# Performance work log

Measured on AMD Instinct MI355X. Metric: run time of the kernel, lower is better.

Reference implementation:

```python
import jax, jax.numpy as jnp
import numpy as np

DMODEL = 1024
NUM_HEADS = 16
HEAD_DIM = DMODEL // NUM_HEADS


def setup_inputs() -> dict:
    key = jax.random.key(0)
    k_x, k_wqkv, k_bqkv, k_wo, k_bo = jax.random.split(key, 5)
    B, T, D = 4, 2048, DMODEL
    s = 1.0 / np.sqrt(D)
    return {
        "x": jax.random.normal(k_x, (B, T, D), dtype=jnp.float32),
        "w_qkv": jax.random.uniform(k_wqkv, (D, 3 * D), dtype=jnp.float32, minval=-s, maxval=s),
        "b_qkv": jax.random.uniform(k_bqkv, (3 * D,), dtype=jnp.float32, minval=-s, maxval=s),
        "w_out": jax.random.uniform(k_wo, (D, D), dtype=jnp.float32, minval=-s, maxval=s),
        "b_out": jax.random.uniform(k_bo, (D,), dtype=jnp.float32, minval=-s, maxval=s),
    }


def reference(x, w_qkv, b_qkv, w_out, b_out):
    B, T, D = x.shape
    H, Hd = NUM_HEADS, HEAD_DIM
    qkv = x @ w_qkv + b_qkv                      # [B,T,3D]
    qkv = qkv.reshape(B, T, 3, H, Hd)
    q = jnp.transpose(qkv[:, :, 0], (0, 2, 1, 3))  # [B,H,T,Hd]
    k = jnp.transpose(qkv[:, :, 1], (0, 2, 1, 3))
    v = jnp.transpose(qkv[:, :, 2], (0, 2, 1, 3))
    scores = jnp.einsum("bhqd,bhkd->bhqk", q, k) / jnp.sqrt(jnp.float32(Hd))
    weights = jax.nn.softmax(scores, axis=-1)
    attn = jnp.einsum("bhqk,bhkd->bhqd", weights, v)  # [B,H,T,Hd]
    attn = jnp.transpose(attn, (0, 2, 1, 3)).reshape(B, T, D)
    return attn @ w_out + b_out
```

## Files before the change

### kernel.cpp

```cpp
#include <hip/hip_runtime.h>
#include <hip/hip_bf16.h>


typedef __bf16 bf16_t;
typedef __bf16 bf16x8 __attribute__((ext_vector_type(8)));
typedef float f32x4 __attribute__((ext_vector_type(4)));
typedef short short4v __attribute__((ext_vector_type(4)));

#if __has_builtin(__builtin_amdgcn_mfma_f32_16x16x16_bf16)
typedef __bf16 bf16x4 __attribute__((ext_vector_type(4)));
#define MFMA_PV(va, vb, c) __builtin_amdgcn_mfma_f32_16x16x16_bf16( \
    __builtin_bit_cast(bf16x4, (va)), __builtin_bit_cast(bf16x4, (vb)), (c), 0, 0, 0)
#else
#define MFMA_PV(va, vb, c) __builtin_amdgcn_mfma_f32_16x16x16bf16_1k((va), (vb), (c), 0, 0, 0)
#endif

#define DMODEL 1024
#define NH     16
#define HD     64
#define BATCH  4
#define SEQ    2048
#define NTOK   (BATCH * SEQ)
#define NOUT   (NTOK * DMODEL)
#define CEXP   0.1803368801111204f

__device__ __forceinline__ void async_ld16(void* lds, const void* g) {
  __builtin_amdgcn_global_load_lds(
      (const __attribute__((address_space(1))) void*)g,
      (__attribute__((address_space(3))) void*)lds, 16, 0, 0);
}

__global__ __launch_bounds__(256) void sniff_dtype(
    const uint4* __restrict__ x, int* __restrict__ flag,
    const void* __restrict__ sq, const void* __restrict__ so,
    float* __restrict__ dq, float* __restrict__ dofs) {
  int t = threadIdx.x;
  int nanish = 0, zc = 0;
  for (int j = 0; j < 4; ++j) {
    uint4 w = x[t + j * 256];
    unsigned u[4] = {w.x, w.y, w.z, w.w};
    for (int k = 0; k < 4; ++k) {
      unsigned lo = u[k] & 0xFFFFu, hi = u[k] >> 16;
      if ((lo & 0x7F80u) == 0x7F80u) nanish++;
      if ((hi & 0x7F80u) == 0x7F80u) nanish++;
      if (lo == 0) zc++;
      if (hi == 0) zc++;
    }
  }
  __shared__ int rn[256], rz[256];
  rn[t] = nanish; rz[t] = zc;
  __syncthreads();
  for (int s = 128; s > 0; s >>= 1) {
    if (t < s) { rn[t] += rn[t + s]; rz[t] += rz[t + s]; }
    __syncthreads();
  }
  const int f = (rn[0] > 4 || rz[0] > 2048) ? 1 : 0;
  if (t == 0) flag[0] = f;
  for (int j = 0; j < 16; ++j) {
    int i = j * 256 + t;
    if (i < 3072)
      dq[i] = f ? ((const float*)sq)[i] : (float)((const bf16_t*)sq)[i];
    else {
      int k = i - 3072;
      dofs[k] = f ? ((const float*)so)[k] : (float)((const bf16_t*)so)[k];
    }
  }
}

__global__ __launch_bounds__(256) void conv_and_transpose(
    const void* __restrict__ x, bf16_t* __restrict__ xb,
    const void* __restrict__ w0, bf16_t* __restrict__ out0,
    const void* __restrict__ w1, bf16_t* __restrict__ out1,
    const int* __restrict__ flag) {
  const int bb = blockIdx.x;
  if (bb < 4096) {
    int i = (bb * 256 + threadIdx.x) * 8;
    if (flag[0]) {
      const float4* s = (const float4*)((const float*)x + i);
      float4 a = s[0], b = s[1];
      bf16_t* o = xb + i;
      o[0] = (bf16_t)a.x; o[1] = (bf16_t)a.y; o[2] = (bf16_t)a.z; o[3] = (bf16_t)a.w;
      o[4] = (bf16_t)b.x; o[5] = (bf16_t)b.y; o[6] = (bf16_t)b.z; o[7] = (bf16_t)b.w;
    } else {
      *(uint4*)(xb + i) = *(const uint4*)((const bf16_t*)x + i);
    }
    return;
  }
  __shared__ bf16_t tile[32][33];
  const int idx = bb - 4096;
  const int bxT = idx & 127, byT = idx >> 7;
  const int tx = threadIdx.x & 31, ty = threadIdx.x >> 5;
  const bool second = bxT >= 96;
  const void* in = second ? w1 : w0;
  bf16_t* out = second ? out1 : out0;
  const int C = second ? 1024 : 3072;
  const int R = 1024;
  const int c0 = (second ? (bxT - 96) : bxT) * 32;
  const int r0 = byT * 32;
  if (flag[0]) {
    for (int i = 0; i < 4; ++i) {
      int r = ty + i * 8;
      tile[r][tx] = (bf16_t)((const float*)in)[(size_t)(r0 + r) * C + c0 + tx];
    }
  } else {
    for (int i = 0; i < 4; ++i) {
      int r = ty + i * 8;
      tile[r][tx] = ((const bf16_t*)in)[(size_t)(r0 + r) * C + c0 + tx];
    }
  }
  __syncthreads();
  for (int i = 0; i < 4; ++i) {
    int r = ty + i * 8;
    out[(size_t)(c0 + r) * R + r0 + tx] = tile[tx][r];
  }
}

template <int MODE>
__global__ __launch_bounds__(512) void gemm_v2(
    const bf16_t* __restrict__ A, const bf16_t* __restrict__ Bt,
    const float* __restrict__ bias, void* __restrict__ Cout,
    int M, int N, int K, bf16_t* __restrict__ vT,
    const int* __restrict__ flag) {
  __shared__ __align__(16) char smem[98304];
  char* lds = smem;
  const int t = threadIdx.x;
  const int wave = t >> 6, lane = t & 63;
  const int quad = lane >> 4, l16 = lane & 15;
  const int wr = wave >> 2, wc = wave & 3;
  const int lin = blockIdx.y * gridDim.x + blockIdx.x;
  const int xcd = lin & 7;
  const int slot = lin >> 3;
  const int Rrows = ((gridDim.x * gridDim.y) >> 3) / gridDim.x;
  const int CW = gridDim.x < 4 ? gridDim.x : 4;
  const int CB = CW * Rrows;
  const int chunk = slot / CB, within = slot % CB;
  const int bx = chunk * CW + within % CW;
  const int by = xcd * Rrows + within / CW;
  const int bM = by * 128, bN = bx * 256;

  const int srow = t >> 2;
  const int xr = ((srow >> 3) & 1) | (((srow >> 2) & 1) << 1);
  const int skl = ((t ^ xr) & 3) * 8;
  const size_t offA = (size_t)(bM + srow) * K + skl;
  const size_t offB = (size_t)(bN + srow) * K + skl;
  const size_t offB2 = offB + (size_t)128 * K;

#define STG(g) do {                                                            \
    const int tile_ = (g) >> 1, half_ = (g) & 1;                               \
    const int kk_ = tile_ * 64 + half_ * 32;                                   \
    char* base_ = lds + ((tile_ & 1) ? 49152 : 0);                             \
    async_ld16(base_ + half_ * 8192 + t * 16, A + offA + kk_);                 \
    async_ld16(base_ + 16384 + half_ * 16384 + t * 16, Bt + offB + kk_);       \
    async_ld16(base_ + 16384 + half_ * 16384 + 8192 + t * 16,                  \
               Bt + offB2 + kk_); } while (0)

  int aoff[4], boff[4];
#pragma unroll
  for (int mf = 0; mf < 4; ++mf) {
    int r = wr * 64 + mf * 16 + l16;
    aoff[mf] = ((r << 6) + (quad << 4)) ^ (((r & 8) << 1) | ((r & 4) << 3));
  }
#pragma unroll
  for (int nf = 0; nf < 4; ++nf) {
    int r = wc * 64 + nf * 16 + l16;
    boff[nf] = ((r << 6) + (quad << 4)) ^ (((r & 8) << 1) | ((r & 4) << 3));
  }

  f32x4 acc[4][4] = {};
  const int NT = K >> 6;

  STG(0); STG(1); STG(2);
  asm volatile("s_waitcnt vmcnt(6)" ::: "memory");
  __builtin_amdgcn_s_barrier();
  asm volatile("" ::: "memory");

#define PHASE(T, h) do {                                                       \
    const int bufo_ = ((T) & 1) * 49152;                                       \
    bf16x8 af[4], bf[4];                                                       \
    _Pragma("unroll") for (int i_ = 0; i_ < 4; ++i_)                           \
      af[i_] = *(const bf16x8*)(lds + bufo_ + (h) * 8192 + aoff[i_]);          \
    _Pragma("unroll") for (int j_ = 0; j_ < 4; ++j_)                           \
      bf[j_] = *(const bf16x8*)(lds + bufo_ + 16384 + (h) * 16384 + boff[j_]); \
    const int n_ = 2 * (T) + (h);                                              \
    if (n_ + 3 < 2 * NT) {                                                     \
      STG(n_ + 3);                                                             \
      asm volatile("s_waitcnt vmcnt(6)" ::: "memory");                         \
    } else if (n_ == 2 * NT - 3) {                                             \
      asm volatile("s_waitcnt vmcnt(3)" ::: "memory");                         \
    } else if (n_ == 2 * NT - 2) {                                             \
      asm volatile("s_waitcnt vmcnt(0)" ::: "memory");                         \
    }                                                                          \
    __builtin_amdgcn_s_barrier();                                              \
    asm volatile("" ::: "memory");                                             \
    __builtin_amdgcn_s_setprio(1);                                             \
    _Pragma("unroll") for (int i_ = 0; i_ < 4; ++i_)                           \
      { _Pragma("unroll") for (int j_ = 0; j_ < 4; ++j_)                       \
        acc[i_][j_] = __builtin_amdgcn_mfma_f32_16x16x32_bf16(                 \
            af[i_], bf[j_], acc[i_][j_], 0, 0, 0); }                           \
    __builtin_amdgcn_s_setprio(0);                                             \
    asm volatile("" ::: "memory");                                             \
    __builtin_amdgcn_s_barrier(); } while (0)

  for (int T = 0; T < NT; ++T) {
    PHASE(T, 0);
    PHASE(T, 1);
  }

  const bool f32out = (MODE == 1) && flag[0];
#pragma unroll
  for (int nf = 0; nf < 4; ++nf) {
    int col = bN + wc * 64 + nf * 16 + l16;
    float bv = bias[col];
#pragma unroll
    for (int mf = 0; mf < 4; ++mf) {
      int row0 = bM + wr * 64 + mf * 16 + quad * 4;
      if (MODE == 2 && col >= 2048) {
        int hh = (col - 2048) >> 6, dd = (col - 2048) & 63;
        bf16_t o4[4];
        for (int r = 0; r < 4; ++r) o4[r] = (bf16_t)(acc[mf][nf][r] + bv);
        size_t dst = ((((size_t)(row0 >> 11) * NH + hh) * HD + dd) << 11) | (row0 & 2047);
        *(uint2*)&vT[dst] = *(uint2*)o4;
      } else if (MODE == 2) {
        float scale = (col < 1024) ? CEXP : 1.0f;
        for (int r = 0; r < 4; ++r)
          ((bf16_t*)Cout)[(size_t)(row0 + r) * N + col] =
              (bf16_t)((acc[mf][nf][r] + bv) * scale);
      } else {
        for (int r = 0; r < 4; ++r) {
          float v = acc[mf][nf][r] + bv;
          if (f32out) ((float*)Cout)[(size_t)(row0 + r) * N + col] = v;
          else        ((bf16_t*)Cout)[(size_t)(row0 + r) * N + col] = (bf16_t)v;
        }
      }
    }
  }
#undef STG
#undef PHASE
}

__global__ __launch_bounds__(512) void attention_v12(
    const bf16_t* __restrict__ qkv, const bf16_t* __restrict__ vT,
    bf16_t* __restrict__ attn) {
  const int t = threadIdx.x;
  const int wave = t >> 6, lane = t & 63;
  const int quad = lane >> 4, l16 = lane & 15;
  const int bh = blockIdx.x, b = bh >> 4, h = bh & 15;
  const int qw = blockIdx.y * 256 + wave * 32;

  __shared__ bf16_t Kt[2][128 * 64];
  __shared__ bf16_t Vt[2][64 * 128];

  const bf16_t* qglob = qkv + (size_t)b * SEQ * 3072 + h * 64;
  const bf16_t* kglob = qglob + 1024;
  const bf16_t* vglob = vT + (size_t)bh * HD * SEQ;

  bf16x8 qf[2][2];
  for (int s = 0; s < 2; ++s) {
    const bf16_t* qrow = qglob + (size_t)(qw + s * 16 + l16) * 3072 + quad * 8;
    qf[s][0] = *(const bf16x8*)qrow;
    qf[s][1] = *(const bf16x8*)(qrow + 32);
  }

  f32x4 accO[2][4] = {};
  f32x4 lsum[2] = {};
  const short4v ones4 = {(short)0x3F80, (short)0x3F80, (short)0x3F80, (short)0x3F80};

  const int kRow = lane >> 3, kSlot = lane & 7;
  const int vRow = lane >> 4, vSlot = lane & 15;

  auto stageKV = [&](int buf, int kt) {
    for (int j = 0; j < 2; ++j) {
      int keyl = wave * 16 + j * 8 + kRow;
      int gc = kSlot ^ (keyl & 7);
      async_ld16((char*)Kt[buf] + (wave * 16 + j * 8) * 128,
                 kglob + (size_t)(kt + keyl) * 3072 + gc * 8);
    }
    for (int j = 0; j < 2; ++j) {
      int d = wave * 8 + j * 4 + vRow;
      int gc = vSlot ^ (d & 15);
      async_ld16((char*)Vt[buf] + (wave * 8 + j * 4) * 256,
                 vglob + (size_t)d * SEQ + kt + gc * 8);
    }
  };

  stageKV(0, 0);

  for (int ti = 0; ti < SEQ / 128; ++ti) {
    const int buf = ti & 1;
    __syncthreads();
    if (ti + 1 < SEQ / 128) stageKV(buf ^ 1, (ti + 1) * 128);

    const bf16_t* KtB = Kt[buf];
    const bf16_t* VtB = Vt[buf];

    for (int kb = 0; kb < 8; ++kb) {
      const bf16_t* kr = &KtB[(kb * 16 + l16) * 64];
      bf16x8 kf0 = *(const bf16x8*)(kr + ((quad ^ (l16 & 7)) * 8));
      bf16x8 kf1 = *(const bf16x8*)(kr + (((4 + quad) ^ (l16 & 7)) * 8));

      short4v pB[2];
      for (int s = 0; s < 2; ++s) {
        f32x4 z = {0.f, 0.f, 0.f, 0.f};
        f32x4 st = __builtin_amdgcn_mfma_f32_16x16x32_bf16(kf0, qf[s][0], z, 0, 0, 0);
        st = __builtin_amdgcn_mfma_f32_16x16x32_bf16(kf1, qf[s][1], st, 0, 0, 0);
        union { bf16_t hh[4]; short4v s4; } u;
        for (int r = 0; r < 4; ++r) {
          float p = __builtin_amdgcn_exp2f(st[r]);
          u.hh[r] = (bf16_t)p;
        }
        pB[s] = u.s4;
        lsum[s] = MFMA_PV(ones4, pB[s], lsum[s]);
      }

      const int chunkbase = kb * 2 + (quad >> 1);
      const int coff = (quad & 1) * 4;
      for (int db = 0; db < 4; ++db) {
        short4v vf = *(const short4v*)&VtB[(db * 16 + l16) * 128 +
                                           ((chunkbase ^ l16) * 8) + coff];
        for (int s = 0; s < 2; ++s)
          accO[s][db] = MFMA_PV(vf, pB[s], accO[s][db]);
      }
    }
  }

  for (int s = 0; s < 2; ++s) {
    float inv = 1.f / lsum[s][0];
    size_t tok = (size_t)b * SEQ + qw + s * 16 + l16;
    for (int db = 0; db < 4; ++db) {
      bf16_t o4[4];
      for (int r = 0; r < 4; ++r) o4[r] = (bf16_t)(accO[s][db][r] * inv);
      *(uint2*)&attn[tok * DMODEL + h * HD + db * 16 + quad * 4] = *(uint2*)o4;
    }
  }
}

extern "C" void kernel_launch(void* const* d_in, const int* in_sizes, int n_in,
                              void* d_out, int out_size, void* d_ws, size_t ws_size,
                              hipStream_t stream) {
  const void* x     = d_in[0];
  const void* w_qkv = d_in[1];
  const void* b_qkv = d_in[2];
  const void* w_out = d_in[3];
  const void* b_out = d_in[4];

  char* ws = (char*)d_ws;
  int*    flag  = (int*)ws;
  bf16_t* wqkvT = (bf16_t*)(ws + 4096);
  bf16_t* woutT = (bf16_t*)(ws + 6295552);
  float*  bqkvf = (float*)(ws + 8392704);
  float*  boutf = (float*)(ws + 8404992);
  bf16_t* qkv   = (bf16_t*)(ws + 8409088);
  bf16_t* xb    = (bf16_t*)(ws + 58740736);
  bf16_t* attn  = xb;
  bf16_t* vTbuf = (bf16_t*)(ws + 75517952);

  sniff_dtype<<<1, 256, 0, stream>>>((const uint4*)x, flag, b_qkv, b_out,
                                     bqkvf, boutf);

  conv_and_transpose<<<8192, 256, 0, stream>>>(x, xb, w_qkv, wqkvT, w_out, woutT,
                                               flag);

  gemm_v2<2><<<dim3(12, 64), 512, 0, stream>>>(
      xb, wqkvT, bqkvf, qkv, NTOK, 3072, 1024, vTbuf, flag);

  attention_v12<<<dim3(BATCH * NH, SEQ / 256), 512, 0, stream>>>(qkv, vTbuf, attn);

  gemm_v2<1><<<dim3(4, 64), 512, 0, stream>>>(
      attn, woutT, boutf, d_out, NTOK, 1024, 1024, nullptr, flag);
}
```

Before: 277.4 us.

## Swap MFMA operands for row-contiguous epilogue stores and split V-projection GEMM

Non-V GEMM modes swap the MFMA A/B operands, so the accumulator holds four consecutive columns per lane. The epilogue can then do vectorized float4 bias loads and 8- or 16-byte stores instead of scattered scalar bf16 stores. The V columns of the QKV projection move to a separate MODE 3 launch that keeps the original operand order, so its transposed vT writes stay vectorized along the sequence axis. This costs one extra kernel launch and a smaller grid per launch.

```diff
diff --git a/kernel.cpp b/kernel.cpp
--- a/kernel.cpp
+++ b/kernel.cpp
@@ -194,9 +194,13 @@
     asm volatile("" ::: "memory");                                             \
     __builtin_amdgcn_s_setprio(1);                                             \
     _Pragma("unroll") for (int i_ = 0; i_ < 4; ++i_)                           \
-      { _Pragma("unroll") for (int j_ = 0; j_ < 4; ++j_)                       \
-        acc[i_][j_] = __builtin_amdgcn_mfma_f32_16x16x32_bf16(                 \
-            af[i_], bf[j_], acc[i_][j_], 0, 0, 0); }                           \
+      { _Pragma("unroll") for (int j_ = 0; j_ < 4; ++j_) {                     \
+        if constexpr (MODE != 3)                                               \
+          acc[i_][j_] = __builtin_amdgcn_mfma_f32_16x16x32_bf16(               \
+              bf[j_], af[i_], acc[i_][j_], 0, 0, 0);                           \
+        else                                                                   \
+          acc[i_][j_] = __builtin_amdgcn_mfma_f32_16x16x32_bf16(               \
+              af[i_], bf[j_], acc[i_][j_], 0, 0, 0); } }                       \
     __builtin_amdgcn_s_setprio(0);                                             \
     asm volatile("" ::: "memory");                                             \
     __builtin_amdgcn_s_barrier(); } while (0)
@@ -206,30 +210,41 @@
     PHASE(T, 1);
   }
 
-  const bool f32out = (MODE == 1) && flag[0];
-#pragma unroll
-  for (int nf = 0; nf < 4; ++nf) {
-    int col = bN + wc * 64 + nf * 16 + l16;
-    float bv = bias[col];
-#pragma unroll
-    for (int mf = 0; mf < 4; ++mf) {
-      int row0 = bM + wr * 64 + mf * 16 + quad * 4;
-      if (MODE == 2 && col >= 2048) {
-        int hh = (col - 2048) >> 6, dd = (col - 2048) & 63;
+  if constexpr (MODE == 3) {
+#pragma unroll
+    for (int nf = 0; nf < 4; ++nf) {
+      int col = bN + wc * 64 + nf * 16 + l16;
+      float bv = bias[col];
+#pragma unroll
+      for (int mf = 0; mf < 4; ++mf) {
+        int row0 = bM + wr * 64 + mf * 16 + quad * 4;
+        int hh = col >> 6, dd = col & 63;
         bf16_t o4[4];
         for (int r = 0; r < 4; ++r) o4[r] = (bf16_t)(acc[mf][nf][r] + bv);
         size_t dst = ((((size_t)(row0 >> 11) * NH + hh) * HD + dd) << 11) | (row0 & 2047);
         *(uint2*)&vT[dst] = *(uint2*)o4;
-      } else if (MODE == 2) {
-        float scale = (col < 1024) ? CEXP : 1.0f;
-        for (int r = 0; r < 4; ++r)
-          ((bf16_t*)Cout)[(size_t)(row0 + r) * N + col] =
-              (bf16_t)((acc[mf][nf][r] + bv) * scale);
-      } else {
-        for (int r = 0; r < 4; ++r) {
-          float v = acc[mf][nf][r] + bv;
-          if (f32out) ((float*)Cout)[(size_t)(row0 + r) * N + col] = v;
-          else        ((bf16_t*)Cout)[(size_t)(row0 + r) * N + col] = (bf16_t)v;
+      }
+    }
+  } else {
+    const bool f32out = (MODE == 1) && flag[0];
+#pragma unroll
+    for (int nf = 0; nf < 4; ++nf) {
+      int ncol0 = bN + wc * 64 + nf * 16 + quad * 4;
+      float4 bv4 = *(const float4*)&bias[ncol0];
+      float sc = (MODE == 2 && ncol0 < 1024) ? CEXP : 1.0f;
+#pragma unroll
+      for (int mf = 0; mf < 4; ++mf) {
+        int mrow = bM + wr * 64 + mf * 16 + l16;
+        float v0 = (acc[mf][nf][0] + bv4.x) * sc;
+        float v1 = (acc[mf][nf][1] + bv4.y) * sc;
+        float v2 = (acc[mf][nf][2] + bv4.z) * sc;
+        float v3 = (acc[mf][nf][3] + bv4.w) * sc;
+        if (f32out) {
+          float4 o = {v0, v1, v2, v3};
+          *(float4*)&((float*)Cout)[(size_t)mrow * N + ncol0] = o;
+        } else {
+          bf16_t o4[4] = {(bf16_t)v0, (bf16_t)v1, (bf16_t)v2, (bf16_t)v3};
+          *(uint2*)&((bf16_t*)Cout)[(size_t)mrow * N + ncol0] = *(uint2*)o4;
         }
       }
     }
@@ -360,8 +375,12 @@
   conv_and_transpose<<<8192, 256, 0, stream>>>(x, xb, w_qkv, wqkvT, w_out, woutT,
                                                flag);
 
-  gemm_v2<2><<<dim3(12, 64), 512, 0, stream>>>(
-      xb, wqkvT, bqkvf, qkv, NTOK, 3072, 1024, vTbuf, flag);
+  gemm_v2<2><<<dim3(8, 64), 512, 0, stream>>>(
+      xb, wqkvT, bqkvf, qkv, NTOK, 3072, 1024, nullptr, flag);
+
+  gemm_v2<3><<<dim3(4, 64), 512, 0, stream>>>(
+      xb, wqkvT + (size_t)2048 * 1024, bqkvf + 2048, qkv, NTOK, 3072, 1024,
+      vTbuf, flag);
 
   attention_v12<<<dim3(BATCH * NH, SEQ / 256), 512, 0, stream>>>(qkv, vTbuf, attn);
 
```

Measured after the change: 285.2 us. 1.03x slower.
